# Optimization experiments

Hardware: AMD Instinct MI355X
Metric: run time of the kernel (lower is better)

The kernel has to match this reference:

```python
import jax, jax.numpy as jnp
import numpy as np

B, N, D = 32, 1024, 64   # batch, n_agents, obs_dim (n_agent_inputs)
H, OUT, K = 128, 8, 16   # gnn_hidden_dim, n_agent_outputs, k_neighbours


def setup_inputs() -> dict:
    key = jax.random.key(0)
    k0, k1, k2, k3 = jax.random.split(key, 4)
    s = lambda d: 1.0 / np.sqrt(d)
    return {
        "agent_observations": jax.random.normal(k0, (B, N, D), jnp.float32),
        "W1": jax.random.normal(k1, (D, H), jnp.float32) * s(D),
        "b1": jnp.zeros((H,), jnp.float32),
        "W2": jax.random.normal(k2, (H, H), jnp.float32) * s(H),
        "b2": jnp.zeros((H,), jnp.float32),
        "W_out": jax.random.normal(k3, (H, OUT), jnp.float32) * s(H),
        "b_out": jnp.zeros((OUT,), jnp.float32),
    }


def _forward(obs, W1, b1, W2, b2, W_out, b_out):
    Bs, Nn, _ = obs.shape
    # active-agent mask, as in torch forward: any nonzero feature
    mask = jnp.any(obs != 0.0, axis=2)               # [B, N] bool
    maskf = mask.astype(obs.dtype)
    pos = obs[:, :, 0:2]                              # pos_indices = slice(0, 2)
    # squared pairwise distances (same ordering as cdist p=2, avoids sqrt-at-0 grads)
    diff = pos[:, :, None, :] - pos[:, None, :, :]    # [B, N, N, 2]
    d2 = jnp.sum(diff * diff, axis=-1)                # [B, N, N]
    valid = mask[:, :, None] & mask[:, None, :]
    d2 = jnp.where(valid, d2, jnp.inf)
    # k+1 nearest (self has distance 0 -> first column), drop self
    _, idx = jax.lax.top_k(-d2, K + 1)                # [B, N, K+1]
    nbr = idx[:, :, 1:]                               # targets of edges source->neighbor
    bidx = jnp.arange(Bs)[:, None, None]
    w = jnp.broadcast_to(maskf[:, :, None], nbr.shape)  # edge valid iff source active
    # GCN symmetric norm (gcn_norm re-adds self-loops on top of the module's
    # explicit self-loops -> diagonal weight 2). deg = in-degree incl. 2*self.
    deg = jnp.zeros((Bs, Nn), obs.dtype).at[bidx, nbr].add(w) + 2.0 * maskf
    dinv = jnp.where(deg > 0, jax.lax.rsqrt(jnp.where(deg > 0, deg, 1.0)), 0.0)

    def gcn(h, W, b):
        y = h @ W                                     # [B, N, H']
        # per-edge messages dinv[src] * y[src], scattered into targets
        z = (dinv[:, :, None] * y)[:, :, None, :] * w[..., None]  # [B, N, K, H']
        agg = jnp.zeros_like(y).at[bidx, nbr].add(z)  # sum over in-edges
        out = dinv[:, :, None] * agg + 2.0 * (dinv * dinv)[:, :, None] * y
        return jnp.tanh(out + b)                      # activation_class = Tanh

    h = gcn(obs, W1, b1)
    h = gcn(h, W2, b2)
    out = h @ W_out + b_out                           # output_mlp
    return out * maskf[:, :, None]                    # zeros for inactive agents


def reference(agent_observations, W1, b1, W2, b2, W_out, b_out):
    return _forward(agent_observations, W1, b1, W2, b2, W_out, b_out)
```

## Files before the change

### kernel.cpp

```cpp
#include <hip/hip_runtime.h>
#include <hip/hip_bf16.h>
#include <math.h>

#define BB 32
#define NN 1024
#define DD 64
#define HH 128
#define KK 16
#define OD 8
#define M_TOT (BB*NN)

typedef unsigned long long u64;

static __device__ __forceinline__ int d2b7(float d2) {
  int v = (int)(__float_as_uint(d2) >> 22) - 200;
  v = v < 0 ? 0 : v;
  return v > 126 ? 126 : v;
}

template <int CIN, bool EMIT_MASK>
__global__ __launch_bounds__(512) void k_gemm(const float* __restrict__ X,
                                              const float* __restrict__ W,
                                              float* __restrict__ Y,
                                              float* __restrict__ maskf,
                                              int* __restrict__ degi,
                                              float2* __restrict__ pxy) {
  __shared__ float Ws[32 * HH];
  __shared__ float Xt[32 * 68];
  __shared__ int rowflag[64];
  __shared__ float2 praw[64];
  const int t = threadIdx.x;
  const size_t rowbase = (size_t)blockIdx.x * 64;

  if (EMIT_MASK && t < 64) rowflag[t] = 0;

  const int c4 = (t & 31) * 4;
  const int r4 = (t >> 5) * 4;

  float acc[4][4] = {{0.f}};

  for (int k0 = 0; k0 < CIN; k0 += 32) {
    __syncthreads();
    {
      const float4* Wt4 = (const float4*)(W + (size_t)k0 * HH);
      ((float4*)Ws)[t]       = Wt4[t];
      ((float4*)Ws)[t + 512] = Wt4[t + 512];
    }
    {
      const int row = t >> 3;
      const int kq  = t & 7;
      float4 v = *(const float4*)(X + (rowbase + row) * CIN + k0 + kq * 4);
      if (EMIT_MASK) {
        if (v.x != 0.f || v.y != 0.f || v.z != 0.f || v.w != 0.f)
          rowflag[row] = 1;
        if (k0 == 0 && kq == 0) praw[row] = make_float2(v.x, v.y);
      }
      Xt[(kq * 4 + 0) * 68 + row] = v.x;
      Xt[(kq * 4 + 1) * 68 + row] = v.y;
      Xt[(kq * 4 + 2) * 68 + row] = v.z;
      Xt[(kq * 4 + 3) * 68 + row] = v.w;
    }
    __syncthreads();
#pragma unroll
    for (int k = 0; k < 32; ++k) {
      const float4 xa = *(const float4*)&Xt[k * 68 + r4];
      const float4 wb = *(const float4*)&Ws[k * HH + c4];
      acc[0][0] += xa.x * wb.x; acc[0][1] += xa.x * wb.y; acc[0][2] += xa.x * wb.z; acc[0][3] += xa.x * wb.w;
      acc[1][0] += xa.y * wb.x; acc[1][1] += xa.y * wb.y; acc[1][2] += xa.y * wb.z; acc[1][3] += xa.y * wb.w;
      acc[2][0] += xa.z * wb.x; acc[2][1] += xa.z * wb.y; acc[2][2] += xa.z * wb.z; acc[2][3] += xa.z * wb.w;
      acc[3][0] += xa.w * wb.x; acc[3][1] += xa.w * wb.y; acc[3][2] += xa.w * wb.z; acc[3][3] += xa.w * wb.w;
    }
  }
#pragma unroll
  for (int i = 0; i < 4; ++i)
    *(float4*)(Y + (rowbase + r4 + i) * HH + c4) =
        make_float4(acc[i][0], acc[i][1], acc[i][2], acc[i][3]);

  if (EMIT_MASK && t < 64) {
    const size_t gr = rowbase + t;
    const int any = rowflag[t];
    maskf[gr] = any ? 1.f : 0.f;
    degi[gr] = 0;
    const float inf = __builtin_inff();
    pxy[gr] = any ? praw[t] : make_float2(inf, inf);
  }
}

__global__ __launch_bounds__(256) void k_topk(const float2* __restrict__ pxy,
                                              const float* __restrict__ maskf,
                                              int* __restrict__ nbr,
                                              int* __restrict__ degi) {
  __shared__ float2 pls[NN];
  __shared__ u64 lst[16][64];
  __shared__ int dcnt[16];
  __shared__ int ccnt[16];

  const int b = blockIdx.x;
  const int t = threadIdx.x;
  const int rl = t >> 4;
  const int s  = t & 15;
  const int row = blockIdx.y * 16 + rl;
  const size_t r = (size_t)b * NN + row;

  {
    const float4* src = (const float4*)(pxy + (size_t)b * NN);
    float4* dst = (float4*)pls;
    dst[t] = src[t];
    dst[t + 256] = src[t + 256];
  }
  if (s == 0) { dcnt[rl] = 0; ccnt[rl] = 0; }
  __syncthreads();

  const bool valid = (maskf[r] != 0.f);
  const float2 pi = pls[row];
  const float xi = pi.x, yi = pi.y;

  unsigned cache[16];
  if (valid) {
#pragma unroll
    for (int q = 0; q < 16; ++q) {
      unsigned pk = 0;
#pragma unroll
      for (int u = 0; u < 4; ++u) {
        const int i = q * 4 + u;
        const int j = s * 64 + ((i + s) & 63);
        const float2 p = pls[j];
        const float dx = __fsub_rn(xi, p.x);
        const float dy = __fsub_rn(yi, p.y);
        const float d2 = __fadd_rn(__fmul_rn(dx, dx), __fmul_rn(dy, dy));
        int bv = d2b7(d2);
        if (j == row) bv = 127;
        pk |= (unsigned)bv << (8 * u);
      }
      cache[q] = pk;
    }
  } else {
#pragma unroll
    for (int q = 0; q < 16; ++q) cache[q] = 0x7F7F7F7Fu;
  }

  int lo = 0, hi = 126, ndef = 0;
#pragma unroll
  for (int it = 0; it < 7; ++it) {
    const int mid = (lo + hi) >> 1;
    const unsigned K = (unsigned)(128 + mid) * 0x01010101u;
    int c = 0;
#pragma unroll
    for (int q = 0; q < 16; ++q)
      c += __popc((K - cache[q]) & 0x80808080u);
#pragma unroll
    for (int off = 1; off < 16; off <<= 1)
      c += __shfl_xor(c, off, 16);
    const bool ge = (c >= 16);
    if (ge) hi = mid;
    else { lo = mid + 1; ndef = c; }
  }
  const int Bstar = lo;
  int need = 16 - ndef;

  int cem = 0;
  if (valid) {
    const unsigned Klo = (unsigned)(127 + Bstar) * 0x01010101u;
    const unsigned Khi = Klo + 0x01010101u;
#pragma unroll
    for (int q = 0; q < 16; ++q) {
      const unsigned w = cache[q];
      const unsigned mLE = (Khi - w) & 0x80808080u;
      if (mLE) {
        const unsigned mLT = (Klo - w) & 0x80808080u;
#pragma unroll
        for (int u = 0; u < 4; ++u) {
          const unsigned bit = 0x80u << (8 * u);
          if (mLE & bit) {
            const int j = s * 64 + ((q * 4 + u + s) & 63);
            if (mLT & bit) {
              const int sl = atomicAdd(&dcnt[rl], 1);
              nbr[r * KK + sl] = j;
              atomicAdd(&degi[b * NN + j], 1);
            } else {
              const float2 p = pls[j];
              const float dx = __fsub_rn(xi, p.x);
              const float dy = __fsub_rn(yi, p.y);
              const float d2 = __fadd_rn(__fmul_rn(dx, dx), __fmul_rn(dy, dy));
              const int sl = atomicAdd(&ccnt[rl], 1);
              if (sl < 64) lst[rl][sl] = ((u64)__float_as_uint(d2) << 10) | (unsigned)j;
              ++cem;
            }
          }
        }
      }
    }
  }
  __syncthreads();

  int cn = cem;
#pragma unroll
  for (int off = 1; off < 16; off <<= 1) cn += __shfl_xor(cn, off, 16);
  cn = cn < 64 ? cn : 64;
  if (!valid) { cn = 0; need = 0; }

  u64 k0 = (s      < cn) ? lst[rl][s]      : ~0ull;
  u64 k1 = (s + 16 < cn) ? lst[rl][s + 16] : ~0ull;
  u64 k2 = (s + 32 < cn) ? lst[rl][s + 32] : ~0ull;
  u64 k3 = (s + 48 < cn) ? lst[rl][s + 48] : ~0ull;

  int e = 0;
  while (__any(e < need)) {
    u64 m01 = k0 < k1 ? k0 : k1;
    u64 m23 = k2 < k3 ? k2 : k3;
    u64 m = m01 < m23 ? m01 : m23;
#pragma unroll
    for (int off = 1; off < 16; off <<= 1) {
      const u64 o = __shfl_xor(m, off, 16);
      m = o < m ? o : m;
    }
    if (e < need) {
      if (k0 == m) k0 = ~0ull;
      else if (k1 == m) k1 = ~0ull;
      else if (k2 == m) k2 = ~0ull;
      else if (k3 == m) k3 = ~0ull;
      if (s == 0) {
        const int j = (int)(m & (u64)(NN - 1));
        nbr[r * KK + ndef + e] = j;
        atomicAdd(&degi[b * NN + j], 1);
      }
    }
    ++e;
  }
}

__global__ __launch_bounds__(1024) void k_graph(const int* __restrict__ degi,
                                                const float* __restrict__ maskf,
                                                const int* __restrict__ nbr,
                                                int* __restrict__ cur,
                                                float* __restrict__ dinv,
                                                int2* __restrict__ rev) {
  __shared__ int wsum[16];
  __shared__ int lcur[NN];
  const int b = blockIdx.x, t = threadIdx.x;
  const int lane = t & 63, w = t >> 6;
  const int r = b * NN + t;
  const int d = degi[r];
  int x = d;
#pragma unroll
  for (int off = 1; off < 64; off <<= 1) {
    int y = __shfl_up(x, off, 64);
    if (lane >= off) x += y;
  }
  if (lane == 63) wsum[w] = x;

  const float m = maskf[r];
  const float deg = (float)d + 2.f * m;
  const float dv = (deg > 0.f) ? (1.f / sqrtf(deg)) : 0.f;
  dinv[r] = dv;
  const float sv = dv * m;

  __syncthreads();
  if (w == 0) {
    int v = (lane < 16) ? wsum[lane] : 0;
#pragma unroll
    for (int off = 1; off < 16; off <<= 1) {
      int y = __shfl_up(v, off, 64);
      if (lane >= off) v += y;
    }
    if (lane < 16) wsum[lane] = v;
  }
  __syncthreads();
  const int start = b * (NN * KK) + (w ? wsum[w - 1] : 0) + x - d;
  lcur[t] = start;
  cur[r] = start;
  __syncthreads();

  if (m != 0.f) {
    const int sb = __float_as_int(sv);
    const int4* n4 = (const int4*)(nbr + (size_t)r * KK);
#pragma unroll
    for (int q = 0; q < 4; ++q) {
      int4 v = n4[q];
      int nb[4] = {v.x, v.y, v.z, v.w};
#pragma unroll
      for (int u = 0; u < 4; ++u) {
        const int pos = atomicAdd(&lcur[nb[u]], 1);
        rev[pos] = make_int2(r, sb);
      }
    }
  }
}

template <bool FUSE_OUT>
__global__ __launch_bounds__(256) void k_gcn(const float* __restrict__ y,
                                             const float* __restrict__ dinv,
                                             const int* __restrict__ degi,
                                             const int* __restrict__ cur,
                                             const int2* __restrict__ rev,
                                             const float* __restrict__ bias,
                                             float* __restrict__ hout,
                                             const float* __restrict__ Wo,
                                             const float* __restrict__ bo,
                                             const float* __restrict__ maskf,
                                             float* __restrict__ out) {
  const int t = threadIdx.x;
  const int r = blockIdx.x * 8 + (t >> 5);
  const int lane = t & 31;
  const int cnt = degi[r];
  const int off = cur[r];
  const float di = dinv[r];

  float4 acc = make_float4(0.f, 0.f, 0.f, 0.f);
  int e = 0;
  for (; e + 2 <= cnt; e += 2) {
    const int2 e0 = rev[off + e];
    const int2 e1 = rev[off + e + 1];
    const float4 y0 = *(const float4*)(y + (size_t)e0.x * HH + lane * 4);
    const float4 y1 = *(const float4*)(y + (size_t)e1.x * HH + lane * 4);
    const float s0 = __int_as_float(e0.y);
    const float s1 = __int_as_float(e1.y);
    acc.x += s0 * y0.x; acc.y += s0 * y0.y; acc.z += s0 * y0.z; acc.w += s0 * y0.w;
    acc.x += s1 * y1.x; acc.y += s1 * y1.y; acc.z += s1 * y1.z; acc.w += s1 * y1.w;
  }
  if (e < cnt) {
    const int2 e0 = rev[off + e];
    const float4 y0 = *(const float4*)(y + (size_t)e0.x * HH + lane * 4);
    const float s0 = __int_as_float(e0.y);
    acc.x += s0 * y0.x; acc.y += s0 * y0.y; acc.z += s0 * y0.z; acc.w += s0 * y0.w;
  }

  const float4 ys = *(const float4*)(y + (size_t)r * HH + lane * 4);
  const float4 bb = *(const float4*)(bias + lane * 4);
  const float t2 = 2.f * di * di;
  float4 h;
  h.x = tanhf(di * acc.x + t2 * ys.x + bb.x);
  h.y = tanhf(di * acc.y + t2 * ys.y + bb.y);
  h.z = tanhf(di * acc.z + t2 * ys.z + bb.z);
  h.w = tanhf(di * acc.w + t2 * ys.w + bb.w);

  if (!FUSE_OUT) {
    *(float4*)(hout + (size_t)r * HH + lane * 4) = h;
  } else {
    const float4* W4 = (const float4*)(Wo + (size_t)lane * 4 * OD);
    float o8[OD];
#pragma unroll
    for (int o = 0; o < OD; ++o) o8[o] = 0.f;
#pragma unroll
    for (int cc = 0; cc < 4; ++cc) {
      const float hc = (cc == 0) ? h.x : (cc == 1) ? h.y : (cc == 2) ? h.z : h.w;
      const float4 wa = W4[cc * 2];
      const float4 wbq = W4[cc * 2 + 1];
      o8[0] += hc * wa.x;  o8[1] += hc * wa.y;  o8[2] += hc * wa.z;  o8[3] += hc * wa.w;
      o8[4] += hc * wbq.x; o8[5] += hc * wbq.y; o8[6] += hc * wbq.z; o8[7] += hc * wbq.w;
    }
#pragma unroll
    for (int offx = 1; offx < 32; offx <<= 1) {
#pragma unroll
      for (int o = 0; o < OD; ++o) o8[o] += __shfl_xor(o8[o], offx, 32);
    }
    if (lane == 0) {
      const float mf = maskf[r];
      const float4 b0 = *(const float4*)(bo);
      const float4 b1 = *(const float4*)(bo + 4);
      float4* orow = (float4*)(out + (size_t)r * OD);
      orow[0] = make_float4((o8[0] + b0.x) * mf, (o8[1] + b0.y) * mf,
                            (o8[2] + b0.z) * mf, (o8[3] + b0.w) * mf);
      orow[1] = make_float4((o8[4] + b1.x) * mf, (o8[5] + b1.y) * mf,
                            (o8[6] + b1.z) * mf, (o8[7] + b1.w) * mf);
    }
  }
}

extern "C" void kernel_launch(void* const* d_in, const int* in_sizes, int n_in,
                              void* d_out, int out_size, void* d_ws, size_t ws_size,
                              hipStream_t stream) {
  (void)in_sizes; (void)n_in; (void)out_size; (void)ws_size;
  const float* obs = (const float*)d_in[0];
  const float* W1  = (const float*)d_in[1];
  const float* b1  = (const float*)d_in[2];
  const float* W2  = (const float*)d_in[3];
  const float* b2  = (const float*)d_in[4];
  const float* Wo  = (const float*)d_in[5];
  const float* bo  = (const float*)d_in[6];
  float* out = (float*)d_out;

  char* ws = (char*)d_ws;
  float* maskf = (float*)(ws);
  int*   degi  = (int*)  (ws + (size_t)(128 << 10));
  float* dinv  = (float*)(ws + (size_t)(256 << 10));
  int*   cur   = (int*)  (ws + (size_t)(384 << 10));
  float2* pxy  = (float2*)(ws + (size_t)(512 << 10));
  int*   nbr   = (int*)  (ws + (size_t)(1u << 20));
  int2*  rev   = (int2*) (ws + (size_t)(3u << 20));
  float* ybuf  = (float*)(ws + (size_t)(7u << 20));
  float* hbuf  = (float*)(ws + (size_t)(23u << 20));

  k_gemm<DD, true><<<M_TOT / 64, 512, 0, stream>>>(obs, W1, ybuf, maskf, degi, pxy);
  k_topk<<<dim3(BB, NN / 16), 256, 0, stream>>>(pxy, maskf, nbr, degi);
  k_graph<<<BB, 1024, 0, stream>>>(degi, maskf, nbr, cur, dinv, rev);
  k_gcn<false><<<M_TOT / 8, 256, 0, stream>>>(ybuf, dinv, degi, cur, rev, b1, hbuf,
                                              nullptr, nullptr, nullptr, nullptr);
  k_gemm<HH, false><<<M_TOT / 64, 512, 0, stream>>>(hbuf, W2, ybuf, nullptr, nullptr, nullptr);
  k_gcn<true><<<M_TOT / 8, 256, 0, stream>>>(ybuf, dinv, degi, cur, rev, b2, nullptr,
                                             Wo, bo, maskf, out);
}
```

Baseline: 155.6 us.

## Stage per-batch feature column slices in LDS for GCN aggregation, split output head

The GCN aggregation now runs one block per (batch, 16-column slice). Each block stages that slice of y for all 1024 nodes in shared memory with a rotated layout, and each thread gathers its in-edges from LDS instead of scattered global loads. The fused output projection becomes a separate k_out kernel that writes h to global and reads it back. The top-k byte cache also moves from 32-bit to 64-bit words and sets the self-distance once instead of comparing per element. Costs are 64KB of LDS per block, low occupancy, a serial per-thread edge loop, and an extra h round trip plus one more launch.

```diff
diff --git a/kernel.cpp b/kernel.cpp
--- a/kernel.cpp
+++ b/kernel.cpp
@@ -115,44 +115,57 @@
   const float2 pi = pls[row];
   const float xi = pi.x, yi = pi.y;
 
-  unsigned cache[16];
+  u64 cc[8];
   if (valid) {
 #pragma unroll
-    for (int q = 0; q < 16; ++q) {
-      unsigned pk = 0;
+    for (int q = 0; q < 8; ++q) {
+      unsigned lo = 0, hiw = 0;
 #pragma unroll
       for (int u = 0; u < 4; ++u) {
-        const int i = q * 4 + u;
+        const int i = q * 8 + u;
         const int j = s * 64 + ((i + s) & 63);
         const float2 p = pls[j];
         const float dx = __fsub_rn(xi, p.x);
         const float dy = __fsub_rn(yi, p.y);
         const float d2 = __fadd_rn(__fmul_rn(dx, dx), __fmul_rn(dy, dy));
-        int bv = d2b7(d2);
-        if (j == row) bv = 127;
-        pk |= (unsigned)bv << (8 * u);
-      }
-      cache[q] = pk;
+        lo |= (unsigned)d2b7(d2) << (8 * u);
+      }
+#pragma unroll
+      for (int u = 0; u < 4; ++u) {
+        const int i = q * 8 + 4 + u;
+        const int j = s * 64 + ((i + s) & 63);
+        const float2 p = pls[j];
+        const float dx = __fsub_rn(xi, p.x);
+        const float dy = __fsub_rn(yi, p.y);
+        const float d2 = __fadd_rn(__fmul_rn(dx, dx), __fmul_rn(dy, dy));
+        hiw |= (unsigned)d2b7(d2) << (8 * u);
+      }
+      cc[q] = (u64)lo | ((u64)hiw << 32);
+    }
+    if (s == (row >> 6)) {
+      const int isf = ((row & 63) - s) & 63;
+      const u64 pbit = 0x7Full << (8 * (isf & 7));
+#pragma unroll
+      for (int q = 0; q < 8; ++q) if (q == (isf >> 3)) cc[q] |= pbit;
     }
   } else {
 #pragma unroll
-    for (int q = 0; q < 16; ++q) cache[q] = 0x7F7F7F7Fu;
+    for (int q = 0; q < 8; ++q) cc[q] = 0x7F7F7F7F7F7F7F7Full;
   }
 
   int lo = 0, hi = 126, ndef = 0;
 #pragma unroll
   for (int it = 0; it < 7; ++it) {
     const int mid = (lo + hi) >> 1;
-    const unsigned K = (unsigned)(128 + mid) * 0x01010101u;
+    const u64 K = (u64)(unsigned)(128 + mid) * 0x0101010101010101ull;
     int c = 0;
 #pragma unroll
-    for (int q = 0; q < 16; ++q)
-      c += __popc((K - cache[q]) & 0x80808080u);
+    for (int q = 0; q < 8; ++q)
+      c += __popcll((K - cc[q]) & 0x8080808080808080ull);
 #pragma unroll
     for (int off = 1; off < 16; off <<= 1)
       c += __shfl_xor(c, off, 16);
-    const bool ge = (c >= 16);
-    if (ge) hi = mid;
+    if (c >= 16) hi = mid;
     else { lo = mid + 1; ndef = c; }
   }
   const int Bstar = lo;
@@ -160,19 +173,19 @@
 
   int cem = 0;
   if (valid) {
-    const unsigned Klo = (unsigned)(127 + Bstar) * 0x01010101u;
-    const unsigned Khi = Klo + 0x01010101u;
-#pragma unroll
-    for (int q = 0; q < 16; ++q) {
-      const unsigned w = cache[q];
-      const unsigned mLE = (Khi - w) & 0x80808080u;
+    const u64 Klo = (u64)(unsigned)(127 + Bstar) * 0x0101010101010101ull;
+    const u64 Khi = Klo + 0x0101010101010101ull;
+#pragma unroll
+    for (int q = 0; q < 8; ++q) {
+      const u64 w = cc[q];
+      const u64 mLE = (Khi - w) & 0x8080808080808080ull;
       if (mLE) {
-        const unsigned mLT = (Klo - w) & 0x80808080u;
-#pragma unroll
-        for (int u = 0; u < 4; ++u) {
-          const unsigned bit = 0x80u << (8 * u);
+        const u64 mLT = (Klo - w) & 0x8080808080808080ull;
+#pragma unroll
+        for (int u = 0; u < 8; ++u) {
+          const u64 bit = 0x80ull << (8 * u);
           if (mLE & bit) {
-            const int j = s * 64 + ((q * 4 + u + s) & 63);
+            const int j = s * 64 + ((q * 8 + u + s) & 63);
             if (mLT & bit) {
               const int sl = atomicAdd(&dcnt[rl], 1);
               nbr[r * KK + sl] = j;
@@ -287,84 +300,122 @@
   }
 }
 
-template <bool FUSE_OUT>
-__global__ __launch_bounds__(256) void k_gcn(const float* __restrict__ y,
-                                             const float* __restrict__ dinv,
-                                             const int* __restrict__ degi,
-                                             const int* __restrict__ cur,
-                                             const int2* __restrict__ rev,
-                                             const float* __restrict__ bias,
-                                             float* __restrict__ hout,
+__global__ __launch_bounds__(1024) void k_gcnc(const float* __restrict__ y,
+                                               const float* __restrict__ dinv,
+                                               const int* __restrict__ degi,
+                                               const int* __restrict__ cur,
+                                               const int2* __restrict__ rev,
+                                               const float* __restrict__ bias,
+                                               float* __restrict__ hout) {
+  __shared__ float4 ych[NN * 4];
+  const int b = blockIdx.x;
+  const int c0 = blockIdx.y * 16;
+  const int t = threadIdx.x;
+
+  {
+    const float* yb = y + (size_t)b * NN * HH + c0;
+#pragma unroll
+    for (int k = 0; k < 4; ++k) {
+      const int idx = t + k * 1024;
+      const int rowq = idx >> 2, cq = idx & 3;
+      ych[rowq * 4 + ((cq + rowq) & 3)] =
+          *(const float4*)(yb + (size_t)rowq * HH + cq * 4);
+    }
+  }
+  __syncthreads();
+
+  const int r = b * NN + t;
+  const int cnt = degi[r];
+  const int off = cur[r];
+  const float di = dinv[r];
+
+  float4 a0 = make_float4(0.f, 0.f, 0.f, 0.f);
+  float4 a1 = a0, a2 = a0, a3 = a0;
+  for (int e = 0; e < cnt; ++e) {
+    const int2 ed = rev[off + e];
+    const int sl = ed.x & (NN - 1);
+    const float se = __int_as_float(ed.y);
+    const int base = sl * 4;
+    const float4 y0 = ych[base + (sl & 3)];
+    const float4 y1 = ych[base + ((sl + 1) & 3)];
+    const float4 y2 = ych[base + ((sl + 2) & 3)];
+    const float4 y3 = ych[base + ((sl + 3) & 3)];
+    a0.x += se * y0.x; a0.y += se * y0.y; a0.z += se * y0.z; a0.w += se * y0.w;
+    a1.x += se * y1.x; a1.y += se * y1.y; a1.z += se * y1.z; a1.w += se * y1.w;
+    a2.x += se * y2.x; a2.y += se * y2.y; a2.z += se * y2.z; a2.w += se * y2.w;
+    a3.x += se * y3.x; a3.y += se * y3.y; a3.z += se * y3.z; a3.w += se * y3.w;
+  }
+
+  const int nb4 = t * 4;
+  const float4 s0 = ych[nb4 + (t & 3)];
+  const float4 s1 = ych[nb4 + ((t + 1) & 3)];
+  const float4 s2 = ych[nb4 + ((t + 2) & 3)];
+  const float4 s3 = ych[nb4 + ((t + 3) & 3)];
+  const float4 b0 = *(const float4*)(bias + c0);
+  const float4 b1 = *(const float4*)(bias + c0 + 4);
+  const float4 b2 = *(const float4*)(bias + c0 + 8);
+  const float4 b3 = *(const float4*)(bias + c0 + 12);
+  const float t2 = 2.f * di * di;
+
+  float4 h0, h1, h2, h3;
+  h0.x = tanhf(di * a0.x + t2 * s0.x + b0.x);
+  h0.y = tanhf(di * a0.y + t2 * s0.y + b0.y);
+  h0.z = tanhf(di * a0.z + t2 * s0.z + b0.z);
+  h0.w = tanhf(di * a0.w + t2 * s0.w + b0.w);
+  h1.x = tanhf(di * a1.x + t2 * s1.x + b1.x);
+  h1.y = tanhf(di * a1.y + t2 * s1.y + b1.y);
+  h1.z = tanhf(di * a1.z + t2 * s1.z + b1.z);
+  h1.w = tanhf(di * a1.w + t2 * s1.w + b1.w);
+  h2.x = tanhf(di * a2.x + t2 * s2.x + b2.x);
+  h2.y = tanhf(di * a2.y + t2 * s2.y + b2.y);
+  h2.z = tanhf(di * a2.z + t2 * s2.z + b2.z);
+  h2.w = tanhf(di * a2.w + t2 * s2.w + b2.w);
+  h3.x = tanhf(di * a3.x + t2 * s3.x + b3.x);
+  h3.y = tanhf(di * a3.y + t2 * s3.y + b3.y);
+  h3.z = tanhf(di * a3.z + t2 * s3.z + b3.z);
+  h3.w = tanhf(di * a3.w + t2 * s3.w + b3.w);
+
+  float4* hrow = (float4*)(hout + (size_t)r * HH + c0);
+  hrow[0] = h0; hrow[1] = h1; hrow[2] = h2; hrow[3] = h3;
+}
+
+__global__ __launch_bounds__(256) void k_out(const float* __restrict__ h,
                                              const float* __restrict__ Wo,
                                              const float* __restrict__ bo,
                                              const float* __restrict__ maskf,
                                              float* __restrict__ out) {
+  __shared__ float Ws[HH * OD];
+  __shared__ float bs[OD];
   const int t = threadIdx.x;
-  const int r = blockIdx.x * 8 + (t >> 5);
-  const int lane = t & 31;
-  const int cnt = degi[r];
-  const int off = cur[r];
-  const float di = dinv[r];
-
-  float4 acc = make_float4(0.f, 0.f, 0.f, 0.f);
-  int e = 0;
-  for (; e + 2 <= cnt; e += 2) {
-    const int2 e0 = rev[off + e];
-    const int2 e1 = rev[off + e + 1];
-    const float4 y0 = *(const float4*)(y + (size_t)e0.x * HH + lane * 4);
-    const float4 y1 = *(const float4*)(y + (size_t)e1.x * HH + lane * 4);
-    const float s0 = __int_as_float(e0.y);
-    const float s1 = __int_as_float(e1.y);
-    acc.x += s0 * y0.x; acc.y += s0 * y0.y; acc.z += s0 * y0.z; acc.w += s0 * y0.w;
-    acc.x += s1 * y1.x; acc.y += s1 * y1.y; acc.z += s1 * y1.z; acc.w += s1 * y1.w;
-  }
-  if (e < cnt) {
-    const int2 e0 = rev[off + e];
-    const float4 y0 = *(const float4*)(y + (size_t)e0.x * HH + lane * 4);
-    const float s0 = __int_as_float(e0.y);
-    acc.x += s0 * y0.x; acc.y += s0 * y0.y; acc.z += s0 * y0.z; acc.w += s0 * y0.w;
-  }
-
-  const float4 ys = *(const float4*)(y + (size_t)r * HH + lane * 4);
-  const float4 bb = *(const float4*)(bias + lane * 4);
-  const float t2 = 2.f * di * di;
-  float4 h;
-  h.x = tanhf(di * acc.x + t2 * ys.x + bb.x);
-  h.y = tanhf(di * acc.y + t2 * ys.y + bb.y);
-  h.z = tanhf(di * acc.z + t2 * ys.z + bb.z);
-  h.w = tanhf(di * acc.w + t2 * ys.w + bb.w);
-
-  if (!FUSE_OUT) {
-    *(float4*)(hout + (size_t)r * HH + lane * 4) = h;
-  } else {
-    const float4* W4 = (const float4*)(Wo + (size_t)lane * 4 * OD);
-    float o8[OD];
-#pragma unroll
-    for (int o = 0; o < OD; ++o) o8[o] = 0.f;
-#pragma unroll
-    for (int cc = 0; cc < 4; ++cc) {
-      const float hc = (cc == 0) ? h.x : (cc == 1) ? h.y : (cc == 2) ? h.z : h.w;
-      const float4 wa = W4[cc * 2];
-      const float4 wbq = W4[cc * 2 + 1];
-      o8[0] += hc * wa.x;  o8[1] += hc * wa.y;  o8[2] += hc * wa.z;  o8[3] += hc * wa.w;
-      o8[4] += hc * wbq.x; o8[5] += hc * wbq.y; o8[6] += hc * wbq.z; o8[7] += hc * wbq.w;
-    }
-#pragma unroll
-    for (int offx = 1; offx < 32; offx <<= 1) {
-#pragma unroll
-      for (int o = 0; o < OD; ++o) o8[o] += __shfl_xor(o8[o], offx, 32);
-    }
-    if (lane == 0) {
-      const float mf = maskf[r];
-      const float4 b0 = *(const float4*)(bo);
-      const float4 b1 = *(const float4*)(bo + 4);
-      float4* orow = (float4*)(out + (size_t)r * OD);
-      orow[0] = make_float4((o8[0] + b0.x) * mf, (o8[1] + b0.y) * mf,
-                            (o8[2] + b0.z) * mf, (o8[3] + b0.w) * mf);
-      orow[1] = make_float4((o8[4] + b1.x) * mf, (o8[5] + b1.y) * mf,
-                            (o8[6] + b1.z) * mf, (o8[7] + b1.w) * mf);
-    }
-  }
+  for (int q = t; q < HH * OD / 4; q += 256) ((float4*)Ws)[q] = ((const float4*)Wo)[q];
+  if (t < OD) bs[t] = bo[t];
+  __syncthreads();
+
+  const size_t r = (size_t)blockIdx.x * 256 + t;
+  const float4* hrow = (const float4*)(h + r * HH);
+  float acc[OD];
+#pragma unroll
+  for (int o = 0; o < OD; ++o) acc[o] = 0.f;
+
+#pragma unroll 4
+  for (int q = 0; q < HH / 4; ++q) {
+    const float4 hv = hrow[q];
+    const float* w = &Ws[(q * 4) * OD];
+#pragma unroll
+    for (int o = 0; o < OD; ++o) acc[o] += hv.x * w[o];
+#pragma unroll
+    for (int o = 0; o < OD; ++o) acc[o] += hv.y * w[OD + o];
+#pragma unroll
+    for (int o = 0; o < OD; ++o) acc[o] += hv.z * w[2 * OD + o];
+#pragma unroll
+    for (int o = 0; o < OD; ++o) acc[o] += hv.w * w[3 * OD + o];
+  }
+  const float mf = maskf[r];
+  float4* orow = (float4*)(out + r * OD);
+  orow[0] = make_float4((acc[0] + bs[0]) * mf, (acc[1] + bs[1]) * mf,
+                        (acc[2] + bs[2]) * mf, (acc[3] + bs[3]) * mf);
+  orow[1] = make_float4((acc[4] + bs[4]) * mf, (acc[5] + bs[5]) * mf,
+                        (acc[6] + bs[6]) * mf, (acc[7] + bs[7]) * mf);
 }
 
 extern "C" void kernel_launch(void* const* d_in, const int* in_sizes, int n_in,
@@ -394,9 +445,8 @@
   k_gemm<DD, true><<<M_TOT / 64, 512, 0, stream>>>(obs, W1, ybuf, maskf, degi, pxy);
   k_topk<<<dim3(BB, NN / 16), 256, 0, stream>>>(pxy, maskf, nbr, degi);
   k_graph<<<BB, 1024, 0, stream>>>(degi, maskf, nbr, cur, dinv, rev);
-  k_gcn<false><<<M_TOT / 8, 256, 0, stream>>>(ybuf, dinv, degi, cur, rev, b1, hbuf,
-                                              nullptr, nullptr, nullptr, nullptr);
+  k_gcnc<<<dim3(BB, HH / 16), 1024, 0, stream>>>(ybuf, dinv, degi, cur, rev, b1, hbuf);
   k_gemm<HH, false><<<M_TOT / 64, 512, 0, stream>>>(hbuf, W2, ybuf, nullptr, nullptr, nullptr);
-  k_gcn<true><<<M_TOT / 8, 256, 0, stream>>>(ybuf, dinv, degi, cur, rev, b2, nullptr,
-                                             Wo, bo, maskf, out);
-}
+  k_gcnc<<<dim3(BB, HH / 16), 1024, 0, stream>>>(ybuf, dinv, degi, cur, rev, b2, hbuf);
+  k_out<<<M_TOT / 256, 256, 0, stream>>>(hbuf, Wo, bo, maskf, out);
+}
```

New measurement: 138.3 us. 1.13x faster.
